# Performance work log

Hardware: AMD Instinct MI355X
Metric: run time of the kernel (lower is better)

The kernel has to match this reference:

```python
import jax, jax.numpy as jnp
import numpy as np


def gcn_conv(x, src, dst, W, b, n_nodes):
    # PyG GCNConv with self-loops and symmetric normalization:
    # out_i = sum_{j->i} (deg_i^-1/2 * deg_j^-1/2) * (x_j @ W) + b
    deg = jax.ops.segment_sum(jnp.ones_like(src, dtype=x.dtype), dst,
                              num_segments=n_nodes)  # >= 1 due to self-loops
    dinv = jax.lax.rsqrt(deg)
    norm = dinv[src] * dinv[dst]                      # [E]
    h = x @ W                                         # [N, out]
    msg = h[src] * norm[:, None]                      # [E, out] gather
    out = jax.ops.segment_sum(msg, dst, num_segments=n_nodes)  # scatter-add
    return out + b


def setup_inputs() -> dict:
    key = jax.random.key(0)
    ks = jax.random.split(key, 4)
    N, E, D_IN, D_H, D_OUT = 100000, 1600000, 32, 64, 16
    x = jax.random.normal(ks[0], (N, D_IN), dtype=jnp.float32)
    edge_index = jax.random.randint(ks[1], (2, E), 0, N, dtype=jnp.int64)
    W1 = jax.random.normal(ks[2], (D_IN, D_H), dtype=jnp.float32) / np.sqrt(D_IN)
    b1 = jnp.zeros((D_H,), dtype=jnp.float32)
    W2 = jax.random.normal(ks[3], (D_H, D_OUT), dtype=jnp.float32) / np.sqrt(D_H)
    b2 = jnp.zeros((D_OUT,), dtype=jnp.float32)
    return {"x": x, "edge_index": edge_index, "W1": W1, "b1": b1,
            "W2": W2, "b2": b2}


def reference(x, edge_index, W1, b1, W2, b2):
    n_nodes = x.shape[0]
    loops = jnp.arange(n_nodes, dtype=edge_index.dtype)
    src = jnp.concatenate([edge_index[0], loops])  # add self-loops
    dst = jnp.concatenate([edge_index[1], loops])
    h = jax.nn.relu(gcn_conv(x, src, dst, W1, b1, n_nodes))
    out = gcn_conv(h, src, dst, W2, b2, n_nodes)
    return out
```

## Files before the change

### kernel.cpp

```cpp
#include <hip/hip_runtime.h>

#define DIN  32
#define DH   64
#define DOUT 16
#define BKT_SHIFT 10
#define BKT_NODES 1024
#define MAXBKT 128
#define PBLK 256

__global__ void k_hist(const int* __restrict__ dst, int* __restrict__ hist,
                       int E, int NBKT) {
    __shared__ int h[MAXBKT];
    int tid = threadIdx.x;
    for (int i = tid; i < NBKT; i += blockDim.x) h[i] = 0;
    __syncthreads();
    int nth = gridDim.x * blockDim.x;
    int EV = E >> 2;
    const int4* d4p = (const int4*)dst;
    for (int v = blockIdx.x * blockDim.x + tid; v < EV; v += nth) {
        int4 d = d4p[v];
        atomicAdd(&h[d.x >> BKT_SHIFT], 1);
        atomicAdd(&h[d.y >> BKT_SHIFT], 1);
        atomicAdd(&h[d.z >> BKT_SHIFT], 1);
        atomicAdd(&h[d.w >> BKT_SHIFT], 1);
    }
    if (blockIdx.x == 0 && tid < (E & 3))
        atomicAdd(&h[dst[(E & ~3) + tid] >> BKT_SHIFT], 1);
    __syncthreads();
    for (int i = tid; i < NBKT; i += blockDim.x)
        hist[i * PBLK + blockIdx.x] = h[i];
}

__global__ void k_scanhist(int* __restrict__ hist, int* __restrict__ bucketBase,
                           int total, int NBKT, int E) {
    __shared__ int s[1024];
    int tid = threadIdx.x;
    int chunk = (total + 1023) >> 10;
    int lo = tid * chunk, hi = min(total, lo + chunk);
    int sum = 0;
    for (int i = lo; i < hi; ++i) sum += hist[i];
    s[tid] = sum;
    __syncthreads();
    for (int off = 1; off < 1024; off <<= 1) {
        int t = (tid >= off) ? s[tid - off] : 0;
        __syncthreads();
        s[tid] += t;
        __syncthreads();
    }
    int run = s[tid] - sum;
    for (int i = lo; i < hi; ++i) {
        int v = hist[i];
        if ((i & (PBLK - 1)) == 0) bucketBase[i / PBLK] = run;
        hist[i] = run;
        run += v;
    }
    if (tid == 0) bucketBase[NBKT] = E;
}

__global__ void k_part(const int* __restrict__ src, const int* __restrict__ dst,
                       const int* __restrict__ hist, int2* __restrict__ pairs,
                       int E, int NBKT) {
    __shared__ int cur[MAXBKT];
    int tid = threadIdx.x;
    for (int i = tid; i < NBKT; i += blockDim.x)
        cur[i] = hist[i * PBLK + blockIdx.x];
    __syncthreads();
    int nth = gridDim.x * blockDim.x;
    int EV = E >> 2;
    const int4* d4p = (const int4*)dst;
    const int4* s4p = (const int4*)src;
    for (int v = blockIdx.x * blockDim.x + tid; v < EV; v += nth) {
        int4 d = d4p[v];
        int4 s = s4p[v];
        int p;
        p = atomicAdd(&cur[d.x >> BKT_SHIFT], 1); pairs[p] = (int2){s.x, d.x};
        p = atomicAdd(&cur[d.y >> BKT_SHIFT], 1); pairs[p] = (int2){s.y, d.y};
        p = atomicAdd(&cur[d.z >> BKT_SHIFT], 1); pairs[p] = (int2){s.z, d.z};
        p = atomicAdd(&cur[d.w >> BKT_SHIFT], 1); pairs[p] = (int2){s.w, d.w};
    }
    if (blockIdx.x == 0 && tid < (E & 3)) {
        int e = (E & ~3) + tid;
        int d = dst[e];
        int p = atomicAdd(&cur[d >> BKT_SHIFT], 1);
        pairs[p] = (int2){src[e], d};
    }
}

__global__ void k_build(const int2* __restrict__ pairs, const int* __restrict__ bucketBase,
                        int* __restrict__ rowStart, int* __restrict__ deg,
                        float* __restrict__ dinv, int* __restrict__ edgeSrc,
                        int N, int NBKT) {
    __shared__ int cnt[BKT_NODES];
    __shared__ int startloc[BKT_NODES];
    __shared__ int s[512];
    int b = blockIdx.x;
    int n_lo = b << BKT_SHIFT;
    int nNodes = min(N - n_lo, BKT_NODES);
    int segBase = bucketBase[b];
    int segLen  = bucketBase[b + 1] - segBase;
    int tid = threadIdx.x;

    for (int i = tid; i < nNodes; i += 512) cnt[i] = 0;
    __syncthreads();
    for (int t = tid; t < segLen; t += 512) {
        int2 pr = pairs[segBase + t];
        atomicAdd(&cnt[pr.y - n_lo], 1);
    }
    __syncthreads();
    int i0 = 2 * tid, i1 = 2 * tid + 1;
    int c0 = (i0 < nNodes) ? cnt[i0] : 0;
    int c1 = (i1 < nNodes) ? cnt[i1] : 0;
    s[tid] = c0 + c1;
    __syncthreads();
    for (int off = 1; off < 512; off <<= 1) {
        int t = (tid >= off) ? s[tid - off] : 0;
        __syncthreads();
        s[tid] += t;
        __syncthreads();
    }
    int excl = s[tid] - (c0 + c1);
    if (i0 < nNodes) startloc[i0] = excl;
    if (i1 < nNodes) startloc[i1] = excl + c0;
    __syncthreads();
    for (int i = tid; i < nNodes; i += 512) {
        int c = cnt[i];
        rowStart[n_lo + i] = segBase + startloc[i];
        deg[n_lo + i]      = c;
        dinv[n_lo + i]     = rsqrtf((float)c + 1.0f);
    }
    __syncthreads();
    for (int i = tid; i < nNodes; i += 512) cnt[i] = startloc[i];
    __syncthreads();
    for (int t = tid; t < segLen; t += 512) {
        int2 pr = pairs[segBase + t];
        int p = atomicAdd(&cnt[pr.y - n_lo], 1);
        edgeSrc[segBase + p] = pr.x;
    }
}

__global__ void k_xg(const float4* __restrict__ x4, const float* __restrict__ dinv,
                     float4* __restrict__ xg4, int N) {
    int t = blockIdx.x * blockDim.x + threadIdx.x;
    if (t < N * 8) {
        float d = dinv[t >> 3];
        float4 v = x4[t];
        v.x *= d; v.y *= d; v.z *= d; v.w *= d;
        xg4[t] = v;
    }
}

__global__ void k_agg1(const int* __restrict__ rowStart, const int* __restrict__ deg,
                       const int* __restrict__ edgeSrc, const float4* __restrict__ xg4,
                       float4* __restrict__ s4, int N) {
    int tid = threadIdx.x;
    int w = tid >> 6, lane = tid & 63;
    int es = lane >> 3, fl = lane & 7;
    int node = blockIdx.x * 4 + w;
    if (node >= N) return;

    int s = rowStart[node], c = deg[node];
    float4 a0 = {0,0,0,0}, a1 = {0,0,0,0}, a2 = {0,0,0,0}, a3 = {0,0,0,0};
    int j0 = 0, j1 = 0, j2 = 0, j3 = 0;
    int o0 = es, o1 = 8 + es, o2 = 16 + es, o3 = 24 + es;
    if (o0 < c) j0 = edgeSrc[s + o0];
    if (o1 < c) j1 = edgeSrc[s + o1];
    if (o2 < c) j2 = edgeSrc[s + o2];
    if (o3 < c) j3 = edgeSrc[s + o3];
    if (o0 < c) a0 = xg4[(size_t)j0 * 8 + fl];
    if (o1 < c) a1 = xg4[(size_t)j1 * 8 + fl];
    if (o2 < c) a2 = xg4[(size_t)j2 * 8 + fl];
    if (o3 < c) a3 = xg4[(size_t)j3 * 8 + fl];
    for (int o = 32 + es; o < c; o += 8) {
        int j = edgeSrc[s + o];
        float4 v = xg4[(size_t)j * 8 + fl];
        a0.x += v.x; a0.y += v.y; a0.z += v.z; a0.w += v.w;
    }
    float4 A;
    A.x = (a0.x + a1.x) + (a2.x + a3.x);
    A.y = (a0.y + a1.y) + (a2.y + a3.y);
    A.z = (a0.z + a1.z) + (a2.z + a3.z);
    A.w = (a0.w + a1.w) + (a2.w + a3.w);
#pragma unroll
    for (int m = 8; m <= 32; m <<= 1) {
        A.x += __shfl_xor(A.x, m);
        A.y += __shfl_xor(A.y, m);
        A.z += __shfl_xor(A.z, m);
        A.w += __shfl_xor(A.w, m);
    }
    if (es == 0) {
        float4 sl = xg4[(size_t)node * 8 + fl];
        A.x += sl.x; A.y += sl.y; A.z += sl.z; A.w += sl.w;
        s4[(size_t)node * 8 + fl] = A;
    }
}

__global__ void k_gemm12(const float* __restrict__ sIn, const float* __restrict__ dinv,
                         const float* __restrict__ b1, const float* __restrict__ W1,
                         const float* __restrict__ W2, float* __restrict__ g2, int N) {
    int node = blockIdx.x * blockDim.x + threadIdx.x;
    if (node >= N) return;

    float sv[DIN];
    const float4* s4 = (const float4*)sIn;
#pragma unroll
    for (int q = 0; q < 8; ++q) {
        float4 v = s4[(size_t)node * 8 + q];
        sv[4 * q + 0] = v.x; sv[4 * q + 1] = v.y;
        sv[4 * q + 2] = v.z; sv[4 * q + 3] = v.w;
    }
    float h[DH];
#pragma unroll
    for (int k = 0; k < DH; ++k) h[k] = 0.f;
#pragma unroll
    for (int d = 0; d < DIN; ++d) {
#pragma unroll
        for (int k = 0; k < DH; ++k) h[k] += sv[d] * W1[d * DH + k];
    }
    float di = dinv[node];
#pragma unroll
    for (int k = 0; k < DH; ++k) h[k] = fmaxf(di * h[k] + b1[k], 0.f);
    float g[DOUT];
#pragma unroll
    for (int k = 0; k < DOUT; ++k) g[k] = 0.f;
#pragma unroll
    for (int d = 0; d < DH; ++d) {
#pragma unroll
        for (int k = 0; k < DOUT; ++k) g[k] += h[d] * W2[d * DOUT + k];
    }
    float4* g2_4 = (float4*)g2;
#pragma unroll
    for (int q = 0; q < 4; ++q) {
        float4 r;
        r.x = di * g[4 * q + 0]; r.y = di * g[4 * q + 1];
        r.z = di * g[4 * q + 2]; r.w = di * g[4 * q + 3];
        g2_4[(size_t)node * 4 + q] = r;
    }
}

__global__ void k_agg2(const int* __restrict__ rowStart, const int* __restrict__ deg,
                       const int* __restrict__ edgeSrc, const float4* __restrict__ g2_4,
                       const float* __restrict__ dinv, const float* __restrict__ b2,
                       float4* __restrict__ out4, int N) {
    int tid = threadIdx.x;
    int w = tid >> 6, lane = tid & 63;
    int es = lane >> 2, fl = lane & 3;
    int node = blockIdx.x * 4 + w;
    if (node >= N) return;

    int s = rowStart[node], c = deg[node];
    float4 a0 = {0,0,0,0}, a1 = {0,0,0,0};
    int j0 = 0, j1 = 0;
    int o0 = es, o1 = 16 + es;
    if (o0 < c) j0 = edgeSrc[s + o0];
    if (o1 < c) j1 = edgeSrc[s + o1];
    if (o0 < c) a0 = g2_4[(size_t)j0 * 4 + fl];
    if (o1 < c) a1 = g2_4[(size_t)j1 * 4 + fl];
    for (int o = 32 + es; o < c; o += 16) {
        int j = edgeSrc[s + o];
        float4 v = g2_4[(size_t)j * 4 + fl];
        a0.x += v.x; a0.y += v.y; a0.z += v.z; a0.w += v.w;
    }
    float4 A;
    A.x = a0.x + a1.x; A.y = a0.y + a1.y; A.z = a0.z + a1.z; A.w = a0.w + a1.w;
#pragma unroll
    for (int m = 4; m <= 32; m <<= 1) {
        A.x += __shfl_xor(A.x, m);
        A.y += __shfl_xor(A.y, m);
        A.z += __shfl_xor(A.z, m);
        A.w += __shfl_xor(A.w, m);
    }
    if (es == 0) {
        float4 sl = g2_4[(size_t)node * 4 + fl];
        A.x += sl.x; A.y += sl.y; A.z += sl.z; A.w += sl.w;
        float d = dinv[node];
        const float4* b2_4 = (const float4*)b2;
        float4 bq = b2_4[fl], r;
        r.x = d * A.x + bq.x; r.y = d * A.y + bq.y;
        r.z = d * A.z + bq.z; r.w = d * A.w + bq.w;
        out4[(size_t)node * 4 + fl] = r;
    }
}

static inline size_t align16(size_t v) { return (v + 15) & ~(size_t)15; }

extern "C" void kernel_launch(void* const* d_in, const int* in_sizes, int n_in,
                              void* d_out, int out_size, void* d_ws, size_t ws_size,
                              hipStream_t stream) {
    const float* x  = (const float*)d_in[0];
    const int*   ei = (const int*)  d_in[1];
    const float* W1 = (const float*)d_in[2];
    const float* b1 = (const float*)d_in[3];
    const float* W2 = (const float*)d_in[4];
    const float* b2 = (const float*)d_in[5];

    int N = in_sizes[0] / DIN;
    int E = in_sizes[1] / 2;
    const int* src = ei;
    const int* dst = ei + E;
    int NBKT = (N + BKT_NODES - 1) >> BKT_SHIFT;

    char* base = (char*)d_ws;
    size_t off = 0;
    int*   hist       = (int*)(base + off);   off = align16(off + (size_t)MAXBKT * PBLK * 4);
    int*   bucketBase = (int*)(base + off);   off = align16(off + (size_t)(MAXBKT + 1) * 4);
    int*   rowStart   = (int*)(base + off);   off = align16(off + (size_t)N * 4);
    int*   deg        = (int*)(base + off);   off = align16(off + (size_t)N * 4);
    float* dinv       = (float*)(base + off); off = align16(off + (size_t)N * 4);
    int*   edgeSrc    = (int*)(base + off);   off = align16(off + (size_t)E * 4);
    float* xg         = (float*)(base + off); off = align16(off + (size_t)N * DIN * 4);
    float* sagg       = (float*)(base + off); off = align16(off + (size_t)N * DIN * 4);
    float* g2         = (float*)(base + off); off = align16(off + (size_t)N * DOUT * 4);
    int2*  pairs      = (int2*)sagg;

    k_hist    <<<PBLK, 256, 0, stream>>>(dst, hist, E, NBKT);
    k_scanhist<<<1, 1024, 0, stream>>>(hist, bucketBase, NBKT * PBLK, NBKT, E);
    k_part    <<<PBLK, 256, 0, stream>>>(src, dst, hist, pairs, E, NBKT);
    k_build   <<<NBKT, 512, 0, stream>>>(pairs, bucketBase, rowStart, deg, dinv,
                                         edgeSrc, N, NBKT);

    k_xg<<<((size_t)N * 8 + 255) / 256, 256, 0, stream>>>((const float4*)x, dinv,
                                                          (float4*)xg, N);
    k_agg1<<<(N + 3) / 4, 256, 0, stream>>>(rowStart, deg, edgeSrc,
                                            (const float4*)xg, (float4*)sagg, N);
    k_gemm12<<<(N + 255) / 256, 256, 0, stream>>>(sagg, dinv, b1, W1, W2, g2, N);
    k_agg2<<<(N + 3) / 4, 256, 0, stream>>>(rowStart, deg, edgeSrc,
                                            (const float4*)g2, dinv, b2,
                                            (float4*)d_out, N);
}
```

Before: 264.3 us.

## Pack edge pairs into 32 bits, shrink buckets, fuse x scaling into build

Edge pairs are packed into one 32-bit word (local dst in the upper bits, 17-bit src in the lower bits) instead of an int2, which halves the partition write and build read traffic. Buckets shrink from 1024 to 512 nodes so there are twice as many build blocks, and each thread now owns one node, which simplifies the scan. The separate k_xg kernel is folded into k_build, removing a launch and a reread of dinv. The packing assumes node ids below 2^17, which holds for this N but would break for larger graphs.

```diff
diff --git a/kernel.cpp b/kernel.cpp
--- a/kernel.cpp
+++ b/kernel.cpp
@@ -3,10 +3,12 @@
 #define DIN  32
 #define DH   64
 #define DOUT 16
-#define BKT_SHIFT 10
-#define BKT_NODES 1024
-#define MAXBKT 128
+#define BKT_SHIFT 9
+#define BKT_NODES 512
+#define MAXBKT 256
 #define PBLK 256
+#define SRC_BITS 17
+#define SRC_MASK ((1u << SRC_BITS) - 1u)
 
 __global__ void k_hist(const int* __restrict__ dst, int* __restrict__ hist,
                        int E, int NBKT) {
@@ -58,7 +60,7 @@
 }
 
 __global__ void k_part(const int* __restrict__ src, const int* __restrict__ dst,
-                       const int* __restrict__ hist, int2* __restrict__ pairs,
+                       const int* __restrict__ hist, unsigned* __restrict__ pairs,
                        int E, int NBKT) {
     __shared__ int cur[MAXBKT];
     int tid = threadIdx.x;
@@ -73,26 +75,32 @@
         int4 d = d4p[v];
         int4 s = s4p[v];
         int p;
-        p = atomicAdd(&cur[d.x >> BKT_SHIFT], 1); pairs[p] = (int2){s.x, d.x};
-        p = atomicAdd(&cur[d.y >> BKT_SHIFT], 1); pairs[p] = (int2){s.y, d.y};
-        p = atomicAdd(&cur[d.z >> BKT_SHIFT], 1); pairs[p] = (int2){s.z, d.z};
-        p = atomicAdd(&cur[d.w >> BKT_SHIFT], 1); pairs[p] = (int2){s.w, d.w};
+        p = atomicAdd(&cur[d.x >> BKT_SHIFT], 1);
+        pairs[p] = ((unsigned)(d.x & (BKT_NODES - 1)) << SRC_BITS) | (unsigned)s.x;
+        p = atomicAdd(&cur[d.y >> BKT_SHIFT], 1);
+        pairs[p] = ((unsigned)(d.y & (BKT_NODES - 1)) << SRC_BITS) | (unsigned)s.y;
+        p = atomicAdd(&cur[d.z >> BKT_SHIFT], 1);
+        pairs[p] = ((unsigned)(d.z & (BKT_NODES - 1)) << SRC_BITS) | (unsigned)s.z;
+        p = atomicAdd(&cur[d.w >> BKT_SHIFT], 1);
+        pairs[p] = ((unsigned)(d.w & (BKT_NODES - 1)) << SRC_BITS) | (unsigned)s.w;
     }
     if (blockIdx.x == 0 && tid < (E & 3)) {
         int e = (E & ~3) + tid;
         int d = dst[e];
         int p = atomicAdd(&cur[d >> BKT_SHIFT], 1);
-        pairs[p] = (int2){src[e], d};
-    }
-}
-
-__global__ void k_build(const int2* __restrict__ pairs, const int* __restrict__ bucketBase,
+        pairs[p] = ((unsigned)(d & (BKT_NODES - 1)) << SRC_BITS) | (unsigned)src[e];
+    }
+}
+
+__global__ void k_build(const unsigned* __restrict__ pairs,
+                        const int* __restrict__ bucketBase,
                         int* __restrict__ rowStart, int* __restrict__ deg,
                         float* __restrict__ dinv, int* __restrict__ edgeSrc,
+                        const float4* __restrict__ x4, float4* __restrict__ xg4,
                         int N, int NBKT) {
     __shared__ int cnt[BKT_NODES];
-    __shared__ int startloc[BKT_NODES];
-    __shared__ int s[512];
+    __shared__ int loc[BKT_NODES];
+    __shared__ int s[BKT_NODES];
     int b = blockIdx.x;
     int n_lo = b << BKT_SHIFT;
     int nNodes = min(N - n_lo, BKT_NODES);
@@ -100,52 +108,37 @@
     int segLen  = bucketBase[b + 1] - segBase;
     int tid = threadIdx.x;
 
-    for (int i = tid; i < nNodes; i += 512) cnt[i] = 0;
-    __syncthreads();
-    for (int t = tid; t < segLen; t += 512) {
-        int2 pr = pairs[segBase + t];
-        atomicAdd(&cnt[pr.y - n_lo], 1);
-    }
-    __syncthreads();
-    int i0 = 2 * tid, i1 = 2 * tid + 1;
-    int c0 = (i0 < nNodes) ? cnt[i0] : 0;
-    int c1 = (i1 < nNodes) ? cnt[i1] : 0;
-    s[tid] = c0 + c1;
-    __syncthreads();
-    for (int off = 1; off < 512; off <<= 1) {
+    cnt[tid] = 0;
+    __syncthreads();
+    for (int t = tid; t < segLen; t += BKT_NODES)
+        atomicAdd(&cnt[pairs[segBase + t] >> SRC_BITS], 1);
+    __syncthreads();
+    int c = cnt[tid];
+    s[tid] = c;
+    __syncthreads();
+    for (int off = 1; off < BKT_NODES; off <<= 1) {
         int t = (tid >= off) ? s[tid - off] : 0;
         __syncthreads();
         s[tid] += t;
         __syncthreads();
     }
-    int excl = s[tid] - (c0 + c1);
-    if (i0 < nNodes) startloc[i0] = excl;
-    if (i1 < nNodes) startloc[i1] = excl + c0;
-    __syncthreads();
-    for (int i = tid; i < nNodes; i += 512) {
-        int c = cnt[i];
-        rowStart[n_lo + i] = segBase + startloc[i];
-        deg[n_lo + i]      = c;
-        dinv[n_lo + i]     = rsqrtf((float)c + 1.0f);
-    }
-    __syncthreads();
-    for (int i = tid; i < nNodes; i += 512) cnt[i] = startloc[i];
-    __syncthreads();
-    for (int t = tid; t < segLen; t += 512) {
-        int2 pr = pairs[segBase + t];
-        int p = atomicAdd(&cnt[pr.y - n_lo], 1);
-        edgeSrc[segBase + p] = pr.x;
-    }
-}
-
-__global__ void k_xg(const float4* __restrict__ x4, const float* __restrict__ dinv,
-                     float4* __restrict__ xg4, int N) {
-    int t = blockIdx.x * blockDim.x + threadIdx.x;
-    if (t < N * 8) {
-        float d = dinv[t >> 3];
-        float4 v = x4[t];
-        v.x *= d; v.y *= d; v.z *= d; v.w *= d;
-        xg4[t] = v;
+    loc[tid] = s[tid] - c;
+    if (tid < nNodes) {
+        rowStart[n_lo + tid] = segBase + (s[tid] - c);
+        deg[n_lo + tid]      = c;
+        dinv[n_lo + tid]     = rsqrtf((float)c + 1.0f);
+    }
+    __syncthreads();
+    for (int i = tid; i < nNodes * 8; i += BKT_NODES) {
+        float dv = rsqrtf((float)cnt[i >> 3] + 1.0f);
+        float4 v = x4[(size_t)n_lo * 8 + i];
+        v.x *= dv; v.y *= dv; v.z *= dv; v.w *= dv;
+        xg4[(size_t)n_lo * 8 + i] = v;
+    }
+    for (int t = tid; t < segLen; t += BKT_NODES) {
+        unsigned pk = pairs[segBase + t];
+        int p = atomicAdd(&loc[pk >> SRC_BITS], 1);
+        edgeSrc[segBase + p] = (int)(pk & SRC_MASK);
     }
 }
 
@@ -310,16 +303,15 @@
     float* xg         = (float*)(base + off); off = align16(off + (size_t)N * DIN * 4);
     float* sagg       = (float*)(base + off); off = align16(off + (size_t)N * DIN * 4);
     float* g2         = (float*)(base + off); off = align16(off + (size_t)N * DOUT * 4);
-    int2*  pairs      = (int2*)sagg;
+    unsigned* pairs   = (unsigned*)sagg;
 
     k_hist    <<<PBLK, 256, 0, stream>>>(dst, hist, E, NBKT);
     k_scanhist<<<1, 1024, 0, stream>>>(hist, bucketBase, NBKT * PBLK, NBKT, E);
     k_part    <<<PBLK, 256, 0, stream>>>(src, dst, hist, pairs, E, NBKT);
-    k_build   <<<NBKT, 512, 0, stream>>>(pairs, bucketBase, rowStart, deg, dinv,
-                                         edgeSrc, N, NBKT);
-
-    k_xg<<<((size_t)N * 8 + 255) / 256, 256, 0, stream>>>((const float4*)x, dinv,
-                                                          (float4*)xg, N);
+    k_build   <<<NBKT, BKT_NODES, 0, stream>>>(pairs, bucketBase, rowStart, deg,
+                                               dinv, edgeSrc, (const float4*)x,
+                                               (float4*)xg, N, NBKT);
+
     k_agg1<<<(N + 3) / 4, 256, 0, stream>>>(rowStart, deg, edgeSrc,
                                             (const float4*)xg, (float4*)sagg, N);
     k_gemm12<<<(N + 255) / 256, 256, 0, stream>>>(sagg, dinv, b1, W1, W2, g2, N);
```

Result: slower. 296.5 us (+12.2%).
